# Kernel tuning notes

Hardware: AMD Instinct MI355X
Metric: run time of the kernel (lower is better)

Reference implementation:

```python
import jax, jax.numpy as jnp
import numpy as np

B, N, D, H, E = 8, 2048, 128, 256, 524288
EPS = 1e-5

def setup_inputs() -> dict:
    key = jax.random.key(0)
    ks = jax.random.split(key, 16)
    def lin(k, fan_in, shape):
        b = 1.0 / np.sqrt(fan_in)
        return jax.random.uniform(k, shape, jnp.float32, -b, b)
    return {
        'x': jax.random.normal(ks[0], (B, N, 3), jnp.float32),
        'h': jax.random.normal(ks[1], (B, N, D), jnp.float32),
        'edge_indices': jax.random.randint(ks[2], (2, E), 0, B * N, jnp.int64),
        'batch_size': B,
        # filter_net: Linear(1,H) -> SiLU -> Linear(H,D)   (weights stored [in,out])
        'W1': lin(ks[3], 1, (1, H)), 'b1': lin(ks[4], 1, (H,)),
        'W2': lin(ks[5], H, (H, D)), 'b2': lin(ks[6], H, (D,)),
        # update_net: Linear(2D,H) -> LayerNorm(H) -> SiLU -> Linear(H,D)
        'W3': lin(ks[7], 2 * D, (2 * D, H)), 'b3': lin(ks[8], 2 * D, (H,)),
        'gamma': jnp.ones((H,), jnp.float32), 'beta': jnp.zeros((H,), jnp.float32),
        'W4': lin(ks[9], H, (H, D)), 'b4': lin(ks[10], H, (D,)),
    }

def reference(x, h, edge_indices, batch_size, W1, b1, W2, b2, W3, b3, gamma, beta, W4, b4):
    Bn, Nn, Dn = h.shape
    row, col = edge_indices[0], edge_indices[1]
    br, nr = row // Nn, row % Nn
    bc, nc = col // Nn, col % Nn
    x_row = x[br, nr]            # [E,3] gather
    x_col = x[bc, nc]            # [E,3]
    h_col = h[bc, nc]            # [E,D]
    diff = x_row - x_col
    dist = jnp.sqrt(jnp.sum(diff * diff, axis=-1, keepdims=True))  # [E,1]
    # distance-conditioned edge filter MLP
    edge_filters = jax.nn.silu(dist @ W1 + b1) @ W2 + b2           # [E,D]
    messages = h_col * edge_filters                                 # [E,D]
    # scatter-mean into B*N nodes (single-pass sum + count, clamp_min(1))
    n_tot = Bn * Nn
    sums = jax.ops.segment_sum(messages, row, num_segments=n_tot)
    counts = jax.ops.segment_sum(jnp.ones_like(row, dtype=messages.dtype), row, num_segments=n_tot)
    agg = (sums / jnp.maximum(counts, 1.0)[:, None]).reshape(Bn, Nn, Dn)
    # update MLP with LayerNorm
    u = jnp.concatenate([h, agg], axis=-1) @ W3 + b3               # [B,N,H]
    mu = jnp.mean(u, axis=-1, keepdims=True)
    var = jnp.mean((u - mu) ** 2, axis=-1, keepdims=True)
    un = (u - mu) * jax.lax.rsqrt(var + EPS) * gamma + beta
    return jax.nn.silu(un) @ W4 + b4                                # [B,N,D]
```

## Files before the change

kernel.cpp:

```cpp
#include <hip/hip_runtime.h>
#include <hip/hip_fp16.h>
#include <math.h>

#define BN_NODES 16384
#define DIM 128
#define HID 256
#define TK 4096
#define TRANGE 32.0f
#define TSTEP (TRANGE / (float)TK)
#define TINV  ((float)TK / TRANGE)
#define LN_EPS 1e-5f
#define EPB 4096
#define NBINS 1024
#define CAPB 768

typedef _Float16 f16x8 __attribute__((ext_vector_type(8)));
typedef __attribute__((ext_vector_type(4))) float f32x4;
typedef __attribute__((ext_vector_type(2))) float floatx2;
typedef __attribute__((ext_vector_type(8))) unsigned short ushort8v;

__device__ __forceinline__ unsigned short f2h(float f) {
    _Float16 h = (_Float16)f;
    return *(unsigned short*)&h;
}
__device__ __forceinline__ __half2 u2h2(unsigned int u) {
    union { unsigned int u; __half2 h; } c; c.u = u; return c.h;
}

__device__ __forceinline__ void acc8(uint2 q, uint4 tv, float* a) {
    floatx2 h01 = __builtin_amdgcn_cvt_pk_f32_fp8((int)q.x, false);
    floatx2 h23 = __builtin_amdgcn_cvt_pk_f32_fp8((int)q.x, true);
    floatx2 h45 = __builtin_amdgcn_cvt_pk_f32_fp8((int)q.y, false);
    floatx2 h67 = __builtin_amdgcn_cvt_pk_f32_fp8((int)q.y, true);
    __half2 t01 = u2h2(tv.x), t23 = u2h2(tv.y), t45 = u2h2(tv.z), t67 = u2h2(tv.w);
    a[0] = fmaf(h01[0], __low2float(t01),  a[0]);
    a[1] = fmaf(h01[1], __high2float(t01), a[1]);
    a[2] = fmaf(h23[0], __low2float(t23),  a[2]);
    a[3] = fmaf(h23[1], __high2float(t23), a[3]);
    a[4] = fmaf(h45[0], __low2float(t45),  a[4]);
    a[5] = fmaf(h45[1], __high2float(t45), a[5]);
    a[6] = fmaf(h67[0], __low2float(t67),  a[6]);
    a[7] = fmaf(h67[1], __high2float(t67), a[7]);
}

__device__ __forceinline__ void edge_one(const unsigned int* lrec, int idx, int dd,
        const unsigned char* __restrict__ xq,
        const unsigned short* __restrict__ Tb, float* a) {
    unsigned int r0 = lrec[idx];
    int c0 = (int)((r0 >> 12) & 0x3FFFu), k0 = (int)(r0 & 0xFFFu);
    uint2 q0 = *(const uint2*)&xq[c0 * DIM + dd];
    uint4 t0 = *(const uint4*)&Tb[k0 * DIM + dd];
    acc8(q0, t0, a);
}

__global__ __launch_bounds__(256) void prep_kernel(
        const float* __restrict__ W1, const float* __restrict__ b1,
        const float* __restrict__ W2, const float* __restrict__ b2,
        const float* __restrict__ W3, const float* __restrict__ W4,
        const float* __restrict__ h, const int* __restrict__ ei,
        const float* __restrict__ x,
        unsigned short* __restrict__ Tb, unsigned short* __restrict__ w3t,
        unsigned short* __restrict__ w4t, unsigned short* __restrict__ xh,
        unsigned char* __restrict__ xq, int* __restrict__ bin_cursor,
        unsigned int* __restrict__ staging, int nE) {
    __shared__ float smem[8 * 256 + 8 * 128];
    int bid = blockIdx.x, t = threadIdx.x;
    if (bid < 512) {
        float* a    = smem;
        float* part = smem + 8 * 256;
        int k0 = bid * 8;
        float w1 = W1[t], bb = b1[t];
#pragma unroll
        for (int k = 0; k < 8; ++k) {
            float dist = ((float)(k0 + k) + 0.5f) * TSTEP;
            float z = dist * w1 + bb;
            a[k * 256 + t] = z / (1.0f + expf(-z));
        }
        __syncthreads();
        int hg = t >> 7, d = t & 127;
        float acc[8] = {0.f,0.f,0.f,0.f,0.f,0.f,0.f,0.f};
        for (int hh = 0; hh < 128; ++hh) {
            int hidx = hg * 128 + hh;
            float w = W2[hidx * DIM + d];
#pragma unroll
            for (int k = 0; k < 8; ++k) acc[k] += a[k * 256 + hidx] * w;
        }
        if (hg == 1) {
#pragma unroll
            for (int k = 0; k < 8; ++k) part[k * 128 + d] = acc[k];
        }
        __syncthreads();
        if (hg == 0) {
            float bd = b2[d];
#pragma unroll
            for (int k = 0; k < 8; ++k)
                Tb[(k0 + k) * DIM + d] = f2h(acc[k] + part[k * 128 + d] + bd);
        }
    } else if (bid < 576) {
        float* s = smem;
        int tid = bid - 512, tr = tid >> 3, tc = tid & 7;
        int lr = t >> 5, lc = t & 31;
#pragma unroll
        for (int rep = 0; rep < 4; ++rep) {
            int k = tr * 32 + rep * 8 + lr, n = tc * 32 + lc;
            s[lc * 33 + rep * 8 + lr] = W3[k * 256 + n];
        }
        __syncthreads();
#pragma unroll
        for (int rep = 0; rep < 4; ++rep) {
            int n = tc * 32 + rep * 8 + lr, k = tr * 32 + lc;
            w3t[n * 256 + k] = f2h(s[(rep * 8 + lr) * 33 + lc]);
        }
    } else if (bid < 608) {
        float* s = smem;
        int tid = bid - 576, tr = tid >> 2, tc = tid & 3;
        int lr = t >> 5, lc = t & 31;
#pragma unroll
        for (int rep = 0; rep < 4; ++rep) {
            int k = tr * 32 + rep * 8 + lr, n = tc * 32 + lc;
            s[lc * 33 + rep * 8 + lr] = W4[k * 128 + n];
        }
        __syncthreads();
#pragma unroll
        for (int rep = 0; rep < 4; ++rep) {
            int n = tc * 32 + rep * 8 + lr, k = tr * 32 + lc;
            w4t[n * 256 + k] = f2h(s[(rep * 8 + lr) * 33 + lc]);
        }
    } else if (bid < 1632) {
        int i0 = (bid - 608) * 2048 + t * 8;
        float4 v0 = *(const float4*)&h[i0];
        float4 v1 = *(const float4*)&h[i0 + 4];
        ushort8v o;
        o[0] = f2h(v0.x); o[1] = f2h(v0.y); o[2] = f2h(v0.z); o[3] = f2h(v0.w);
        o[4] = f2h(v1.x); o[5] = f2h(v1.y); o[6] = f2h(v1.z); o[7] = f2h(v1.w);
        *(ushort8v*)&xh[i0] = o;
        unsigned int q0 = 0, q1 = 0;
        q0 = __builtin_amdgcn_cvt_pk_fp8_f32(v0.x, v0.y, q0, false);
        q0 = __builtin_amdgcn_cvt_pk_fp8_f32(v0.z, v0.w, q0, true);
        q1 = __builtin_amdgcn_cvt_pk_fp8_f32(v1.x, v1.y, q1, false);
        q1 = __builtin_amdgcn_cvt_pk_fp8_f32(v1.z, v1.w, q1, true);
        uint2 qq; qq.x = q0; qq.y = q1;
        *(uint2*)&xq[i0] = qq;
    } else {
        __shared__ int cnt[NBINS];
        __shared__ int pre[NBINS];
        __shared__ int gba[NBINS];
        __shared__ int sc[256];
        __shared__ unsigned int rec[EPB];
        int e0 = (bid - 1632) * EPB;
        int m = min(EPB, nE - e0);
        if (m < 0) m = 0;
#pragma unroll
        for (int j = 0; j < 4; ++j) cnt[j * 256 + t] = 0;
        __syncthreads();
        unsigned int code[16];
        int rk[16], bn[16];
#pragma unroll
        for (int j = 0; j < 16; ++j) {
            int idx = j * 256 + t;
            rk[j] = -1; bn[j] = 0; code[j] = 0;
            if (idx < m) {
                int e = e0 + idx;
                int r = ei[e], c = ei[nE + e];
                code[j] = ((unsigned int)r << 14) | (unsigned int)c;
                bn[j] = r >> 4;
                rk[j] = atomicAdd(&cnt[bn[j]], 1);
            }
        }
        __syncthreads();
        int c4[4], s4 = 0;
#pragma unroll
        for (int j = 0; j < 4; ++j) { c4[j] = cnt[t * 4 + j]; s4 += c4[j]; }
        sc[t] = s4;
        __syncthreads();
        for (int off = 1; off < 256; off <<= 1) {
            int v = (t >= off) ? sc[t - off] : 0;
            __syncthreads();
            sc[t] += v;
            __syncthreads();
        }
        int run = sc[t] - s4;
#pragma unroll
        for (int j = 0; j < 4; ++j) {
            int b = t * 4 + j;
            pre[b] = run; run += c4[j];
            gba[b] = atomicAdd(&bin_cursor[b], c4[j]);
        }
        __syncthreads();
#pragma unroll
        for (int j = 0; j < 16; ++j)
            if (rk[j] >= 0) rec[pre[bn[j]] + rk[j]] = code[j];
        __syncthreads();
        for (int i = t; i < m; i += 256) {
            unsigned int cd = rec[i];
            int b = (int)(cd >> 18);
            int r = (int)(cd >> 14);
            int c = (int)(cd & 0x3FFFu);
            float dx = x[r * 3 + 0] - x[c * 3 + 0];
            float dy = x[r * 3 + 1] - x[c * 3 + 1];
            float dz = x[r * 3 + 2] - x[c * 3 + 2];
            float u = sqrtf(dx * dx + dy * dy + dz * dz) * TINV;
            int k = min((int)u, TK - 1);
            unsigned int o = ((unsigned int)(r & 15) << 26)
                           | ((unsigned int)c << 12) | (unsigned int)k;
            int off = gba[b] + (i - pre[b]);
            if (off < CAPB) staging[b * CAPB + off] = o;
        }
    }
}

__global__ __launch_bounds__(512, 4) void mega_kernel(
        const unsigned int* __restrict__ staging, const int* __restrict__ bin_cursor,
        const unsigned short* __restrict__ Tb, const unsigned char* __restrict__ xq,
        const unsigned short* __restrict__ xh, const unsigned short* __restrict__ w3t,
        const float* __restrict__ b3, const float* __restrict__ gamma,
        const float* __restrict__ beta, const unsigned short* __restrict__ w4t,
        const float* __restrict__ b4, float* __restrict__ out) {
    __shared__ unsigned int lrec[CAPB];
    __shared__ int cnt16[16];
    __shared__ int pref[17];
    __shared__ int cur[16];
    __shared__ __align__(16) unsigned short aggh[16][136];
    __shared__ __align__(16) unsigned short a_lds[16][264];
    __shared__ float part_s[8][16], part_q[8][16];
    __shared__ float tot_mu[16], tot_rs[16];

    int t = threadIdx.x;
    int bin = blockIdx.x;
    int n0 = bin * 16;
    long base = (long)bin * CAPB;

    unsigned int sr0 = __builtin_nontemporal_load(&staging[base + t]);
    unsigned int sr1 = __builtin_nontemporal_load(&staging[base + min(t + 512, CAPB - 1)]);
    int total = min(bin_cursor[bin], CAPB);

    if (t < 16) cnt16[t] = 0;
    __syncthreads();

    int have0 = (t < total), have1 = (t + 512 < total);
    if (have0) atomicAdd(&cnt16[sr0 >> 26], 1);
    if (have1) atomicAdd(&cnt16[sr1 >> 26], 1);
    __syncthreads();
    if (t < 16) {
        int c = cnt16[t];
        int s = c;
#pragma unroll
        for (int off = 1; off < 16; off <<= 1) {
            int v = __shfl_up(s, off, 16);
            if (t >= off) s += v;
        }
        pref[t + 1] = s;
        cur[t] = s - c;
        if (t == 0) pref[0] = 0;
    }
    __syncthreads();

    if (have0) { int pos = atomicAdd(&cur[sr0 >> 26], 1); lrec[pos] = sr0; }
    if (have1) { int pos = atomicAdd(&cur[sr1 >> 26], 1); lrec[pos] = sr1; }
    __syncthreads();

    int wid = t >> 6, lane = t & 63;
    int wv = wid, q = lane >> 4, l15 = lane & 15;

    float b3v[2], gv[2], bvv[2];
#pragma unroll
    for (int nt = 0; nt < 2; ++nt) {
        int col = wv * 32 + nt * 16 + l15;
        b3v[nt] = b3[col]; gv[nt] = gamma[col]; bvv[nt] = beta[col];
    }
    float b4v = b4[wv * 16 + l15];
    f16x8 a16[4];
#pragma unroll
    for (int kc = 0; kc < 4; ++kc)
        a16[kc] = *(const f16x8*)&xh[(n0 + l15) * DIM + kc * 32 + q * 8];

    {
        int g = lane >> 4, l16 = lane & 15, dd = l16 * 8;
        int node = wid * 2 + (g >> 1);
        int sub = g & 1;
        int off = pref[node], len = pref[node + 1] - off;
        float a[8] = {0.f,0.f,0.f,0.f,0.f,0.f,0.f,0.f};
        int i = sub;
        for (; i + 6 < len; i += 8) {
            unsigned int r0 = lrec[off + i];
            unsigned int r1 = lrec[off + i + 2];
            unsigned int r2 = lrec[off + i + 4];
            unsigned int r3 = lrec[off + i + 6];
            int c0 = (int)((r0 >> 12) & 0x3FFFu), k0 = (int)(r0 & 0xFFFu);
            int c1 = (int)((r1 >> 12) & 0x3FFFu), k1 = (int)(r1 & 0xFFFu);
            int c2 = (int)((r2 >> 12) & 0x3FFFu), k2 = (int)(r2 & 0xFFFu);
            int c3 = (int)((r3 >> 12) & 0x3FFFu), k3 = (int)(r3 & 0xFFFu);
            uint2 q0 = *(const uint2*)&xq[c0 * DIM + dd];
            uint4 t0 = *(const uint4*)&Tb[k0 * DIM + dd];
            uint2 q1 = *(const uint2*)&xq[c1 * DIM + dd];
            uint4 t1 = *(const uint4*)&Tb[k1 * DIM + dd];
            uint2 q2 = *(const uint2*)&xq[c2 * DIM + dd];
            uint4 t2 = *(const uint4*)&Tb[k2 * DIM + dd];
            uint2 q3 = *(const uint2*)&xq[c3 * DIM + dd];
            uint4 t3 = *(const uint4*)&Tb[k3 * DIM + dd];
            acc8(q0, t0, a);
            acc8(q1, t1, a);
            acc8(q2, t2, a);
            acc8(q3, t3, a);
        }
        for (; i < len; i += 2)
            edge_one(lrec, off + i, dd, xq, Tb, a);
#pragma unroll
        for (int r = 0; r < 8; ++r) a[r] += __shfl_xor(a[r], 16, 64);
        if (sub == 0) {
            float inv = 1.0f / (float)max(len, 1);
            ushort8v o;
#pragma unroll
            for (int r = 0; r < 8; ++r) o[r] = f2h(a[r] * inv);
            *(ushort8v*)&aggh[node][dd] = o;
        }
    }
    __syncthreads();

    f32x4 acc[2];
    acc[0] = (f32x4){0.f, 0.f, 0.f, 0.f};
    acc[1] = (f32x4){0.f, 0.f, 0.f, 0.f};
#pragma unroll
    for (int kc = 0; kc < 8; ++kc) {
        f16x8 a;
        if (kc < 4) a = a16[kc];
        else        a = *(const f16x8*)&aggh[l15][(kc - 4) * 32 + q * 8];
#pragma unroll
        for (int nt = 0; nt < 2; ++nt) {
            f16x8 b = *(const f16x8*)&w3t[(wv * 32 + nt * 16 + l15) * 256 + kc * 32 + q * 8];
            acc[nt] = __builtin_amdgcn_mfma_f32_16x16x32_f16(a, b, acc[nt], 0, 0, 0);
        }
    }

    {
        float s_[4], q_[4];
#pragma unroll
        for (int reg = 0; reg < 4; ++reg) {
            float su = 0.f, sq = 0.f;
#pragma unroll
            for (int nt = 0; nt < 2; ++nt) {
                float v = acc[nt][reg] + b3v[nt];
                acc[nt][reg] = v;
                su += v; sq += v * v;
            }
            s_[reg] = su; q_[reg] = sq;
        }
#pragma unroll
        for (int off = 1; off < 16; off <<= 1) {
#pragma unroll
            for (int reg = 0; reg < 4; ++reg) {
                s_[reg] += __shfl_xor(s_[reg], off, 64);
                q_[reg] += __shfl_xor(q_[reg], off, 64);
            }
        }
        if (l15 == 0) {
#pragma unroll
            for (int reg = 0; reg < 4; ++reg) {
                int r = q * 4 + reg;
                part_s[wv][r] = s_[reg];
                part_q[wv][r] = q_[reg];
            }
        }
    }
    __syncthreads();
    if (t < 16) {
        float st = 0.f, qt = 0.f;
#pragma unroll
        for (int w = 0; w < 8; ++w) { st += part_s[w][t]; qt += part_q[w][t]; }
        float mu = st * (1.0f / 256.0f);
        float var = qt * (1.0f / 256.0f) - mu * mu;
        tot_mu[t] = mu;
        tot_rs[t] = rsqrtf(var + LN_EPS);
    }
    __syncthreads();

#pragma unroll
    for (int reg = 0; reg < 4; ++reg) {
        int r = q * 4 + reg;
        float mu = tot_mu[r], rs = tot_rs[r];
#pragma unroll
        for (int nt = 0; nt < 2; ++nt) {
            float un = (acc[nt][reg] - mu) * rs * gv[nt] + bvv[nt];
            float act = un / (1.0f + expf(-un));
            a_lds[r][wv * 32 + nt * 16 + l15] = f2h(act);
        }
    }
    __syncthreads();

    f32x4 acc2 = (f32x4){0.f, 0.f, 0.f, 0.f};
    int col2 = wv * 16 + l15;
#pragma unroll
    for (int kc = 0; kc < 8; ++kc) {
        f16x8 a = *(const f16x8*)&a_lds[l15][kc * 32 + q * 8];
        f16x8 b = *(const f16x8*)&w4t[col2 * 256 + kc * 32 + q * 8];
        acc2 = __builtin_amdgcn_mfma_f32_16x16x32_f16(a, b, acc2, 0, 0, 0);
    }
#pragma unroll
    for (int reg = 0; reg < 4; ++reg) {
        int node = n0 + q * 4 + reg;
        __builtin_nontemporal_store(acc2[reg] + b4v, &out[node * DIM + col2]);
    }
}

extern "C" void kernel_launch(void* const* d_in, const int* in_sizes, int n_in,
                              void* d_out, int out_size, void* d_ws, size_t ws_size,
                              hipStream_t stream) {
    const float* x     = (const float*)d_in[0];
    const float* h     = (const float*)d_in[1];
    const int*   ei    = (const int*)d_in[2];
    const float* W1    = (const float*)d_in[4];
    const float* b1    = (const float*)d_in[5];
    const float* W2    = (const float*)d_in[6];
    const float* b2    = (const float*)d_in[7];
    const float* W3    = (const float*)d_in[8];
    const float* b3    = (const float*)d_in[9];
    const float* gamma = (const float*)d_in[10];
    const float* beta  = (const float*)d_in[11];
    const float* W4    = (const float*)d_in[12];
    const float* b4    = (const float*)d_in[13];
    float* out = (float*)d_out;
    int nE = in_sizes[2] / 2;

    char* ws = (char*)d_ws;
    unsigned short* Tb   = (unsigned short*)ws; ws += (size_t)TK * DIM * 2;
    unsigned short* w3t  = (unsigned short*)ws; ws += (size_t)HID * HID * 2;
    unsigned short* w4t  = (unsigned short*)ws; ws += (size_t)DIM * HID * 2;
    unsigned short* xh   = (unsigned short*)ws; ws += (size_t)BN_NODES * DIM * 2;
    unsigned char*  xq   = (unsigned char*)ws;  ws += (size_t)BN_NODES * DIM;
    int* bin_cursor = (int*)ws;                 ws += (size_t)NBINS * 4;
    unsigned int* staging = (unsigned int*)ws;  ws += (size_t)NBINS * CAPB * 4;

    int binBlocks = (nE + EPB - 1) / EPB;
    hipMemsetAsync(bin_cursor, 0, (size_t)NBINS * 4, stream);
    prep_kernel<<<1632 + binBlocks, 256, 0, stream>>>(W1, b1, W2, b2, W3, W4, h, ei, x,
                                                      Tb, w3t, w4t, xh, xq,
                                                      bin_cursor, staging, nE);
    mega_kernel<<<NBINS, 512, 0, stream>>>(staging, bin_cursor, Tb, xq, xh,
                                           w3t, b3, gamma, beta, w4t, b4, out);
}
```

Measured before the change: 159.4 us.

## Replace two-level edge binning with per-node atomic slot scatter

Drops the block-local counting sort in prep and the in-block 16-node re-sort in the main kernel. Each edge instead atomically claims a slot in a fixed-capacity per-node staging row. The xh half of the first GEMM is also issued before the aggregation phase so it can overlap with the staging loads. This trades LDS sorting and barriers for one global atomic and one scattered store per edge, and it silently drops edges beyond 80 per node.

```diff
diff --git a/kernel.cpp b/kernel.cpp
--- a/kernel.cpp
+++ b/kernel.cpp
@@ -10,9 +10,9 @@
 #define TSTEP (TRANGE / (float)TK)
 #define TINV  ((float)TK / TRANGE)
 #define LN_EPS 1e-5f
-#define EPB 4096
-#define NBINS 1024
-#define CAPB 768
+#define EPB 2048
+#define NBLK 1024
+#define CAPN 80
 
 typedef _Float16 f16x8 __attribute__((ext_vector_type(8)));
 typedef __attribute__((ext_vector_type(4))) float f32x4;
@@ -43,10 +43,10 @@
     a[7] = fmaf(h67[1], __high2float(t67), a[7]);
 }
 
-__device__ __forceinline__ void edge_one(const unsigned int* lrec, int idx, int dd,
+__device__ __forceinline__ void edge_one(const unsigned int* row, int idx, int dd,
         const unsigned char* __restrict__ xq,
         const unsigned short* __restrict__ Tb, float* a) {
-    unsigned int r0 = lrec[idx];
+    unsigned int r0 = row[idx];
     int c0 = (int)((r0 >> 12) & 0x3FFFu), k0 = (int)(r0 & 0xFFFu);
     uint2 q0 = *(const uint2*)&xq[c0 * DIM + dd];
     uint4 t0 = *(const uint4*)&Tb[k0 * DIM + dd];
@@ -61,7 +61,7 @@
         const float* __restrict__ x,
         unsigned short* __restrict__ Tb, unsigned short* __restrict__ w3t,
         unsigned short* __restrict__ w4t, unsigned short* __restrict__ xh,
-        unsigned char* __restrict__ xq, int* __restrict__ bin_cursor,
+        unsigned char* __restrict__ xq, int* __restrict__ node_cursor,
         unsigned int* __restrict__ staging, int nE) {
     __shared__ float smem[8 * 256 + 8 * 128];
     int bid = blockIdx.x, t = threadIdx.x;
@@ -142,84 +142,32 @@
         uint2 qq; qq.x = q0; qq.y = q1;
         *(uint2*)&xq[i0] = qq;
     } else {
-        __shared__ int cnt[NBINS];
-        __shared__ int pre[NBINS];
-        __shared__ int gba[NBINS];
-        __shared__ int sc[256];
-        __shared__ unsigned int rec[EPB];
         int e0 = (bid - 1632) * EPB;
         int m = min(EPB, nE - e0);
-        if (m < 0) m = 0;
-#pragma unroll
-        for (int j = 0; j < 4; ++j) cnt[j * 256 + t] = 0;
-        __syncthreads();
-        unsigned int code[16];
-        int rk[16], bn[16];
-#pragma unroll
-        for (int j = 0; j < 16; ++j) {
-            int idx = j * 256 + t;
-            rk[j] = -1; bn[j] = 0; code[j] = 0;
-            if (idx < m) {
-                int e = e0 + idx;
-                int r = ei[e], c = ei[nE + e];
-                code[j] = ((unsigned int)r << 14) | (unsigned int)c;
-                bn[j] = r >> 4;
-                rk[j] = atomicAdd(&cnt[bn[j]], 1);
-            }
-        }
-        __syncthreads();
-        int c4[4], s4 = 0;
-#pragma unroll
-        for (int j = 0; j < 4; ++j) { c4[j] = cnt[t * 4 + j]; s4 += c4[j]; }
-        sc[t] = s4;
-        __syncthreads();
-        for (int off = 1; off < 256; off <<= 1) {
-            int v = (t >= off) ? sc[t - off] : 0;
-            __syncthreads();
-            sc[t] += v;
-            __syncthreads();
-        }
-        int run = sc[t] - s4;
-#pragma unroll
-        for (int j = 0; j < 4; ++j) {
-            int b = t * 4 + j;
-            pre[b] = run; run += c4[j];
-            gba[b] = atomicAdd(&bin_cursor[b], c4[j]);
-        }
-        __syncthreads();
-#pragma unroll
-        for (int j = 0; j < 16; ++j)
-            if (rk[j] >= 0) rec[pre[bn[j]] + rk[j]] = code[j];
-        __syncthreads();
         for (int i = t; i < m; i += 256) {
-            unsigned int cd = rec[i];
-            int b = (int)(cd >> 18);
-            int r = (int)(cd >> 14);
-            int c = (int)(cd & 0x3FFFu);
+            int e = e0 + i;
+            int r = ei[e], c = ei[nE + e];
             float dx = x[r * 3 + 0] - x[c * 3 + 0];
             float dy = x[r * 3 + 1] - x[c * 3 + 1];
             float dz = x[r * 3 + 2] - x[c * 3 + 2];
             float u = sqrtf(dx * dx + dy * dy + dz * dz) * TINV;
             int k = min((int)u, TK - 1);
-            unsigned int o = ((unsigned int)(r & 15) << 26)
-                           | ((unsigned int)c << 12) | (unsigned int)k;
-            int off = gba[b] + (i - pre[b]);
-            if (off < CAPB) staging[b * CAPB + off] = o;
+            int off = atomicAdd(&node_cursor[r], 1);
+            if (off < CAPN)
+                staging[(long)r * CAPN + off] = ((unsigned int)c << 12) | (unsigned int)k;
         }
     }
 }
 
 __global__ __launch_bounds__(512, 4) void mega_kernel(
-        const unsigned int* __restrict__ staging, const int* __restrict__ bin_cursor,
+        const unsigned int* __restrict__ staging, const int* __restrict__ node_cursor,
         const unsigned short* __restrict__ Tb, const unsigned char* __restrict__ xq,
         const unsigned short* __restrict__ xh, const unsigned short* __restrict__ w3t,
         const float* __restrict__ b3, const float* __restrict__ gamma,
         const float* __restrict__ beta, const unsigned short* __restrict__ w4t,
         const float* __restrict__ b4, float* __restrict__ out) {
-    __shared__ unsigned int lrec[CAPB];
-    __shared__ int cnt16[16];
-    __shared__ int pref[17];
-    __shared__ int cur[16];
+    __shared__ unsigned int lrec[16][CAPN];
+    __shared__ int lenc[16];
     __shared__ __align__(16) unsigned short aggh[16][136];
     __shared__ __align__(16) unsigned short a_lds[16][264];
     __shared__ float part_s[8][16], part_q[8][16];
@@ -228,36 +176,7 @@
     int t = threadIdx.x;
     int bin = blockIdx.x;
     int n0 = bin * 16;
-    long base = (long)bin * CAPB;
-
-    unsigned int sr0 = __builtin_nontemporal_load(&staging[base + t]);
-    unsigned int sr1 = __builtin_nontemporal_load(&staging[base + min(t + 512, CAPB - 1)]);
-    int total = min(bin_cursor[bin], CAPB);
-
-    if (t < 16) cnt16[t] = 0;
-    __syncthreads();
-
-    int have0 = (t < total), have1 = (t + 512 < total);
-    if (have0) atomicAdd(&cnt16[sr0 >> 26], 1);
-    if (have1) atomicAdd(&cnt16[sr1 >> 26], 1);
-    __syncthreads();
-    if (t < 16) {
-        int c = cnt16[t];
-        int s = c;
-#pragma unroll
-        for (int off = 1; off < 16; off <<= 1) {
-            int v = __shfl_up(s, off, 16);
-            if (t >= off) s += v;
-        }
-        pref[t + 1] = s;
-        cur[t] = s - c;
-        if (t == 0) pref[0] = 0;
-    }
-    __syncthreads();
-
-    if (have0) { int pos = atomicAdd(&cur[sr0 >> 26], 1); lrec[pos] = sr0; }
-    if (have1) { int pos = atomicAdd(&cur[sr1 >> 26], 1); lrec[pos] = sr1; }
-    __syncthreads();
+    if (t < 16) lenc[t] = min(node_cursor[n0 + t], CAPN);
 
     int wid = t >> 6, lane = t & 63;
     int wv = wid, q = lane >> 4, l15 = lane & 15;
@@ -269,23 +188,41 @@
         b3v[nt] = b3[col]; gv[nt] = gamma[col]; bvv[nt] = beta[col];
     }
     float b4v = b4[wv * 16 + l15];
-    f16x8 a16[4];
-#pragma unroll
-    for (int kc = 0; kc < 4; ++kc)
-        a16[kc] = *(const f16x8*)&xh[(n0 + l15) * DIM + kc * 32 + q * 8];
+
+    f32x4 acc[2];
+    acc[0] = (f32x4){0.f, 0.f, 0.f, 0.f};
+    acc[1] = (f32x4){0.f, 0.f, 0.f, 0.f};
+#pragma unroll
+    for (int kc = 0; kc < 4; ++kc) {
+        f16x8 a = *(const f16x8*)&xh[(n0 + l15) * DIM + kc * 32 + q * 8];
+#pragma unroll
+        for (int nt = 0; nt < 2; ++nt) {
+            f16x8 b = *(const f16x8*)&w3t[(wv * 32 + nt * 16 + l15) * 256 + kc * 32 + q * 8];
+            acc[nt] = __builtin_amdgcn_mfma_f32_16x16x32_f16(a, b, acc[nt], 0, 0, 0);
+        }
+    }
+    __syncthreads();
+
+    int j0 = wid * 2, j1 = j0 + 1;
+    int len0 = lenc[j0], len1 = lenc[j1];
+    for (int s = lane; s < len0; s += 64)
+        lrec[j0][s] = staging[(long)(n0 + j0) * CAPN + s];
+    for (int s = lane; s < len1; s += 64)
+        lrec[j1][s] = staging[(long)(n0 + j1) * CAPN + s];
 
     {
         int g = lane >> 4, l16 = lane & 15, dd = l16 * 8;
-        int node = wid * 2 + (g >> 1);
+        int node = j0 + (g >> 1);
         int sub = g & 1;
-        int off = pref[node], len = pref[node + 1] - off;
+        int len = (g >> 1) ? len1 : len0;
+        const unsigned int* lp = lrec[node];
         float a[8] = {0.f,0.f,0.f,0.f,0.f,0.f,0.f,0.f};
         int i = sub;
         for (; i + 6 < len; i += 8) {
-            unsigned int r0 = lrec[off + i];
-            unsigned int r1 = lrec[off + i + 2];
-            unsigned int r2 = lrec[off + i + 4];
-            unsigned int r3 = lrec[off + i + 6];
+            unsigned int r0 = lp[i];
+            unsigned int r1 = lp[i + 2];
+            unsigned int r2 = lp[i + 4];
+            unsigned int r3 = lp[i + 6];
             int c0 = (int)((r0 >> 12) & 0x3FFFu), k0 = (int)(r0 & 0xFFFu);
             int c1 = (int)((r1 >> 12) & 0x3FFFu), k1 = (int)(r1 & 0xFFFu);
             int c2 = (int)((r2 >> 12) & 0x3FFFu), k2 = (int)(r2 & 0xFFFu);
@@ -304,7 +241,7 @@
             acc8(q3, t3, a);
         }
         for (; i < len; i += 2)
-            edge_one(lrec, off + i, dd, xq, Tb, a);
+            edge_one(lp, i, dd, xq, Tb, a);
 #pragma unroll
         for (int r = 0; r < 8; ++r) a[r] += __shfl_xor(a[r], 16, 64);
         if (sub == 0) {
@@ -317,14 +254,9 @@
     }
     __syncthreads();
 
-    f32x4 acc[2];
-    acc[0] = (f32x4){0.f, 0.f, 0.f, 0.f};
-    acc[1] = (f32x4){0.f, 0.f, 0.f, 0.f};
-#pragma unroll
-    for (int kc = 0; kc < 8; ++kc) {
-        f16x8 a;
-        if (kc < 4) a = a16[kc];
-        else        a = *(const f16x8*)&aggh[l15][(kc - 4) * 32 + q * 8];
+#pragma unroll
+    for (int kc = 4; kc < 8; ++kc) {
+        f16x8 a = *(const f16x8*)&aggh[l15][(kc - 4) * 32 + q * 8];
 #pragma unroll
         for (int nt = 0; nt < 2; ++nt) {
             f16x8 b = *(const f16x8*)&w3t[(wv * 32 + nt * 16 + l15) * 256 + kc * 32 + q * 8];
@@ -427,14 +359,14 @@
     unsigned short* w4t  = (unsigned short*)ws; ws += (size_t)DIM * HID * 2;
     unsigned short* xh   = (unsigned short*)ws; ws += (size_t)BN_NODES * DIM * 2;
     unsigned char*  xq   = (unsigned char*)ws;  ws += (size_t)BN_NODES * DIM;
-    int* bin_cursor = (int*)ws;                 ws += (size_t)NBINS * 4;
-    unsigned int* staging = (unsigned int*)ws;  ws += (size_t)NBINS * CAPB * 4;
+    int* node_cursor = (int*)ws;                ws += (size_t)BN_NODES * 4;
+    unsigned int* staging = (unsigned int*)ws;  ws += (size_t)BN_NODES * CAPN * 4;
 
     int binBlocks = (nE + EPB - 1) / EPB;
-    hipMemsetAsync(bin_cursor, 0, (size_t)NBINS * 4, stream);
+    hipMemsetAsync(node_cursor, 0, (size_t)BN_NODES * 4, stream);
     prep_kernel<<<1632 + binBlocks, 256, 0, stream>>>(W1, b1, W2, b2, W3, W4, h, ei, x,
                                                       Tb, w3t, w4t, xh, xq,
-                                                      bin_cursor, staging, nE);
-    mega_kernel<<<NBINS, 512, 0, stream>>>(staging, bin_cursor, Tb, xq, xh,
-                                           w3t, b3, gamma, beta, w4t, b4, out);
-}
+                                                      node_cursor, staging, nE);
+    mega_kernel<<<NBLK, 512, 0, stream>>>(staging, node_cursor, Tb, xq, xh,
+                                          w3t, b3, gamma, beta, w4t, b4, out);
+}
```

After: 165.6 us. +3.9%, slower.
